# Kernel optimization log

Hardware: AMD Instinct MI355X
Metric: run time of the kernel (lower is better)

The kernel has to match this reference:

```python
import jax, jax.numpy as jnp
import numpy as np

B_IN = 30    # input sphere bandwidth
B_MID = 16   # bandwidth after S2 conv
B_OUT = 10   # bandwidth after SO3 conv
F0, F1 = 100, 100
NUM_CLS = 40
EPS = 1e-5


def _wigner_d(l, betas):
    """Real Wigner-d matrices d^l_{mn}(beta) -> [len(betas), 2l+1, 2l+1] (numpy)."""
    betas = np.asarray(betas, np.float64)
    n = 2 * l + 1
    if l == 0:
        return np.ones((betas.size, 1, 1))
    m = np.arange(-l, l)
    c = np.sqrt(l * (l + 1) - m * (m + 1))      # <m+1|J+|m>
    Jp = np.zeros((n, n)); Jp[np.arange(1, n), np.arange(n - 1)] = c
    K = -(Jp - Jp.T) / 2.0                      # K = -i*Jy, real antisymmetric; d = exp(beta*K)
    w, V = np.linalg.eigh(1j * K)
    ph = np.exp(-1j * np.outer(betas, w))
    return np.einsum('ij,bj,kj->bik', V, ph, V.conj()).real


def _dh(b):
    """Driscoll-Healy beta samples and quadrature weights for bandwidth b."""
    k = np.arange(2 * b)
    beta = np.pi * (2 * k + 1) / (4 * b)
    j = np.arange(b)
    w = (2.0 / b) * np.sin(beta) * (np.sin(np.outer(2 * k + 1, 2 * j + 1) * np.pi / (4 * b)) @ (1.0 / (2 * j + 1)))
    return beta, w


def _project(x, b):
    """Point cloud [B,3,N] -> radial distance image on S2 grid [B,1,2b,2b] (beta, alpha)."""
    nb = 2 * b
    r = jnp.linalg.norm(x, axis=1)                                   # [B,N]
    beta = jnp.arccos(jnp.clip(x[:, 2] / jnp.maximum(r, 1e-8), -1.0, 1.0))
    alpha = jnp.mod(jnp.arctan2(x[:, 1], x[:, 0]), 2.0 * np.pi)
    bi = jnp.clip((beta / np.pi * nb).astype(jnp.int32), 0, nb - 1)
    ai = jnp.clip((alpha / (2.0 * np.pi) * nb).astype(jnp.int32), 0, nb - 1)
    Bb = x.shape[0]
    flat = (jnp.arange(Bb)[:, None] * nb * nb + bi * nb + ai).reshape(-1)
    img = jnp.zeros((Bb * nb * nb,), x.dtype).at[flat].max(r.reshape(-1))
    return img.reshape(Bb, 1, nb, nb)


def _s2_fft(x, b_out):
    """x [B,C,2b,2b] (beta,alpha) -> list over l of fhat^l_m [B,C,2l+1] complex."""
    N = x.shape[-1]
    beta, qw = _dh(N // 2)
    G = jnp.fft.fft(x.astype(jnp.complex64), axis=-1)                # coeff of e^{-im alpha}
    out = []
    for l in range(b_out):
        d0 = _wigner_d(l, beta)[:, :, l]                             # d^l_{m,0}(beta_k)
        wd = jnp.asarray(qw[:, None] * d0 * (2 * np.pi / N), jnp.complex64)
        mi = np.arange(-l, l + 1) % N
        out.append(jnp.einsum('km,bckm->bcm', wd, G[..., mi]))
    return out


def _s2_rft(w, b_out, n_alpha):
    """Dirac kernel on equatorial S2 grid (beta=pi/2) -> list over l of [f_in,f_out,2l+1]."""
    alphas = 2 * np.pi * np.arange(n_alpha) / n_alpha
    wc = w.astype(jnp.complex64) / n_alpha
    out = []
    for l in range(b_out):
        m = np.arange(-l, l + 1)
        basis = _wigner_d(l, [np.pi / 2])[0][:, l][:, None] * np.exp(-1j * np.outer(m, alphas))
        out.append(jnp.einsum('mp,iop->iom', jnp.asarray(basis, jnp.complex64), wc))
    return out


def _so3_fft(x, b_out):
    """x [B,C,2b,2b,2b] (beta,alpha,gamma) -> list over l of [B,C,2l+1,2l+1]."""
    N = x.shape[-1]
    beta, qw = _dh(N // 2)
    G = jnp.fft.fft2(x.astype(jnp.complex64), axes=(-2, -1))
    out = []
    for l in range(b_out):
        d = _wigner_d(l, beta)
        wd = jnp.asarray(qw[:, None, None] * d * (2 * np.pi / N) ** 2, jnp.complex64)
        mi = np.arange(-l, l + 1) % N
        out.append(jnp.einsum('kmn,bckmn->bcmn', wd, G[..., mi[:, None], mi[None, :]]))
    return out


def _so3_rft(w, b_out, n_alpha):
    """Dirac kernel on equatorial SO3 grid (beta=pi/2, gamma=0) -> list of [f_in,f_out,2l+1,2l+1]."""
    alphas = 2 * np.pi * np.arange(n_alpha) / n_alpha
    wc = w.astype(jnp.complex64) / n_alpha
    out = []
    for l in range(b_out):
        m = np.arange(-l, l + 1)
        d = _wigner_d(l, [np.pi / 2])[0]
        basis = d[None] * np.exp(-1j * np.outer(alphas, m))[:, :, None]   # [P,2l+1,2l+1]
        out.append(jnp.einsum('pmn,iop->iomn', jnp.asarray(basis, jnp.complex64), wc))
    return out


def _so3_ifft(Z, b_out):
    """Spectral blocks (list over l of [B,f,2l+1,2l+1]) -> x [B,f,2b,2b,2b] real."""
    N = 2 * b_out
    beta, _ = _dh(b_out)
    Bb, f = Z[0].shape[:2]
    M = jnp.zeros((Bb, f, N, N, N), jnp.complex64)
    for l, Zl in enumerate(Z):
        d = jnp.asarray((2 * l + 1) * _wigner_d(l, beta), jnp.complex64)
        mi = np.arange(-l, l + 1) % N
        M = M.at[:, :, :, mi[:, None], mi[None, :]].add(jnp.einsum('kmn,bfmn->bfkmn', d, Zl))
    return (jnp.fft.ifft2(M, axes=(-2, -1)) * (N * N)).real


def _bn_relu(x, g, b):
    mu = x.mean(axis=(0, 2, 3, 4), keepdims=True)
    var = ((x - mu) ** 2).mean(axis=(0, 2, 3, 4), keepdims=True)
    y = (x - mu) * jax.lax.rsqrt(var + EPS) * g[None, :, None, None, None] + b[None, :, None, None, None]
    return jax.nn.relu(y)


def _so3_integrate(x):
    b = x.shape[-1] // 2
    _, qw = _dh(b)
    return jnp.einsum('bfkag,k->bf', x, jnp.asarray(qw, x.dtype)) * (2 * np.pi / (2 * b)) ** 2


def _forward(x, w_s2, bias_s2, bn1_g, bn1_b, w_so3, bias_so3, bn2_g, bn2_b, lin_w, lin_b):
    img = _project(x, B_IN)                                   # [B,1,60,60]
    X = _s2_fft(img, B_MID)
    Y = _s2_rft(w_s2, B_MID, 2 * B_IN)
    # correlation theorem on S2: Z^l_{mn} = sum_i X^l_{i,m} conj(Y^l_{i,n})
    Z = [jnp.einsum('bim,ion->bomn', Xl, jnp.conj(Yl)) for Xl, Yl in zip(X, Y)]
    h = _so3_ifft(Z, B_MID) + bias_s2[None, :, None, None, None]   # [B,100,32,32,32]
    h = _bn_relu(h, bn1_g, bn1_b)
    X2 = _so3_fft(h, B_OUT)
    Y2 = _so3_rft(w_so3, B_OUT, 2 * B_MID)
    # correlation theorem on SO3: Z^l = X^l @ Y^l^dagger (feature-contracted)
    Z2 = [jnp.einsum('bimk,ionk->bomn', Xl, jnp.conj(Yl)) for Xl, Yl in zip(X2, Y2)]
    h2 = _so3_ifft(Z2, B_OUT) + bias_so3[None, :, None, None, None]  # [B,100,20,20,20]
    h2 = _bn_relu(h2, bn2_g, bn2_b)
    feat = _so3_integrate(h2)                                 # [B,100]
    return feat @ lin_w + lin_b                               # cls_logits [B,40]


def setup_inputs() -> dict:
    key = jax.random.key(0)
    ks = jax.random.split(key, 4)
    B, Np = 8, 1024
    return {
        'x': jax.random.normal(ks[0], (B, 3, Np), jnp.float32),
        'w_s2': jax.random.normal(ks[1], (1, F0, 2 * B_IN), jnp.float32) * 0.1,
        'bias_s2': jnp.zeros((F0,), jnp.float32),
        'bn1_g': jnp.ones((F0,), jnp.float32),
        'bn1_b': jnp.zeros((F0,), jnp.float32),
        'w_so3': jax.random.normal(ks[2], (F0, F1, 2 * B_MID), jnp.float32) * 0.1,
        'bias_so3': jnp.zeros((F1,), jnp.float32),
        'bn2_g': jnp.ones((F1,), jnp.float32),
        'bn2_b': jnp.zeros((F1,), jnp.float32),
        'lin_w': jax.random.normal(ks[3], (F1, NUM_CLS), jnp.float32) * 0.1,
        'lin_b': jnp.zeros((NUM_CLS,), jnp.float32),
    }


def reference(x, w_s2, bias_s2, bn1_g, bn1_b, w_so3, bias_so3, bn2_g, bn2_b, lin_w, lin_b):
    return _forward(x, w_s2, bias_s2, bn1_g, bn1_b, w_so3, bias_so3, bn2_g, bn2_b, lin_w, lin_b)
```

## Files before the change

### kernel.cpp

```cpp
#include <hip/hip_runtime.h>
#include <math.h>

#ifndef M_PI
#define M_PI 3.14159265358979323846
#endif

#define TBL_MAGIC 0x5EED5EEDCAFEF00DULL

__device__ const int c_off2[11] = {0,1,10,35,84,165,286,455,680,969,1330};
__device__ const int c_offH[11] = {0,1,7,22,50,95,161,252,372,525,715};
__device__ const int c_T[17] = {0,1,3,6,10,15,21,28,36,45,55,66,78,91,105,120,136};

__device__ constexpr float CS32[32] = {
  1.0f, 0.98078528f, 0.92387953f, 0.83146961f, 0.70710678f, 0.55557023f, 0.38268343f, 0.19509032f,
  0.0f,-0.19509032f,-0.38268343f,-0.55557023f,-0.70710678f,-0.83146961f,-0.92387953f,-0.98078528f,
 -1.0f,-0.98078528f,-0.92387953f,-0.83146961f,-0.70710678f,-0.55557023f,-0.38268343f,-0.19509032f,
  0.0f, 0.19509032f, 0.38268343f, 0.55557023f, 0.70710678f, 0.83146961f, 0.92387953f, 0.98078528f};
__device__ constexpr float SN32[32] = {
  0.0f, 0.19509032f, 0.38268343f, 0.55557023f, 0.70710678f, 0.83146961f, 0.92387953f, 0.98078528f,
  1.0f, 0.98078528f, 0.92387953f, 0.83146961f, 0.70710678f, 0.55557023f, 0.38268343f, 0.19509032f,
  0.0f,-0.19509032f,-0.38268343f,-0.55557023f,-0.70710678f,-0.83146961f,-0.92387953f,-0.98078528f,
 -1.0f,-0.98078528f,-0.92387953f,-0.83146961f,-0.70710678f,-0.55557023f,-0.38268343f,-0.19509032f};

__device__ __forceinline__ int l_from_sq(int off){ int l=0; while((l+1)*(l+1)<=off) l++; return l; }
__device__ __forceinline__ int l_from_offH(int off){ int l=0; while(c_offH[l+1]<=off) l++; return l; }
__device__ __forceinline__ int l_from_T(int c){ int l=0; while(c_T[l+1]<=c) l++; return l; }

__global__ void k_delta(double* Dd, float* Df, const unsigned long long* __restrict__ tflag){
  if (tflag[0]==TBL_MAGIC) return;
  int l = blockIdx.x; int n = 2*l+1; int n2=n*n;
  __shared__ double A[961], T[961], Tm[961];
  for (int idx=threadIdx.x; idx<n2; idx+=1024){
    int r=idx/n, c=idx-r*n;
    double v=0.0;
    if (r==c+1){ double m=(double)(c-l); v = -0.5*sqrt((double)l*(l+1)-m*(m+1)); }
    else if (c==r+1){ double m=(double)(r-l); v = 0.5*sqrt((double)l*(l+1)-m*(m+1)); }
    A[idx] = v*(M_PI*0.5/128.0);
    T[idx] = (r==c)?1.0:0.0;
  }
  __syncthreads();
  for (int j=14; j>=1; --j){
    for (int idx=threadIdx.x; idx<n2; idx+=1024){
      int r=idx/n, c=idx-r*n; double acc=0.0;
      if (r>0)   acc += A[r*n+(r-1)]*T[(r-1)*n+c];
      if (r<n-1) acc += A[r*n+(r+1)]*T[(r+1)*n+c];
      Tm[idx]=acc;
    }
    __syncthreads();
    for (int idx=threadIdx.x; idx<n2; idx+=1024){
      int r=idx/n, c=idx-r*n;
      T[idx] = ((r==c)?1.0:0.0) + Tm[idx]/(double)j;
    }
    __syncthreads();
  }
  for (int s=0; s<7; ++s){
    for (int idx=threadIdx.x; idx<n2; idx+=1024){
      int r=idx/n, c=idx-r*n; double acc=0.0;
      for (int q=0;q<n;q++) acc += T[r*n+q]*T[q*n+c];
      Tm[idx]=acc;
    }
    __syncthreads();
    for (int idx=threadIdx.x; idx<n2; idx+=1024) T[idx]=Tm[idx];
    __syncthreads();
  }
  for (int idx=threadIdx.x; idx<n2; idx+=1024){ Dd[l*961+idx]=T[idx]; Df[l*961+idx]=(float)T[idx]; }
}

__global__ void k_qw(float* qw30, float* qw16, float* qw10, float2* ph32, float2* ph20, float2* ph60,
                     const unsigned long long* __restrict__ tflag){
  if (tflag[0]==TBL_MAGIC) return;
  int t=threadIdx.x;
  if (t<60){
    double beta=M_PI*(2*t+1)/120.0, s=0.0;
    for (int j=0;j<30;j++) s += sin((double)(2*t+1)*(2*j+1)*M_PI/120.0)/(double)(2*j+1);
    qw30[t]=(float)((2.0/30.0)*sin(beta)*s);
    double a=2.0*M_PI*t/60.0; ph60[t]=make_float2((float)cos(a),(float)sin(a));
  }
  if (t<32){
    double beta=M_PI*(2*t+1)/64.0, s=0.0;
    for (int j=0;j<16;j++) s += sin((double)(2*t+1)*(2*j+1)*M_PI/64.0)/(double)(2*j+1);
    qw16[t]=(float)((2.0/16.0)*sin(beta)*s);
    double a=2.0*M_PI*t/32.0; ph32[t]=make_float2((float)cos(a),(float)sin(a));
  }
  if (t<20){
    double beta=M_PI*(2*t+1)/40.0, s=0.0;
    for (int j=0;j<10;j++) s += sin((double)(2*t+1)*(2*j+1)*M_PI/40.0)/(double)(2*j+1);
    qw10[t]=(float)((2.0/10.0)*sin(beta)*s);
    double a=2.0*M_PI*t/20.0; ph20[t]=make_float2((float)cos(a),(float)sin(a));
  }
}

__global__ void k_tables(const double* Dd, const float* qw30, const float* qw16, const float* qw10,
                         float* wd_s2, float* dif16, float* wd16, float* dif10,
                         const unsigned long long* __restrict__ tflag){
  if (tflag[0]==TBL_MAGIC) return;
  int bid=blockIdx.x;
  __shared__ double cc[32], ss[32];
  int l,k,mode; double beta;
  if (bid<960){ mode=0; l=bid/60; k=bid%60; beta=M_PI*(2*k+1)/120.0; }
  else if (bid<1472){ mode=1; int q=bid-960; l=q/32; k=q%32; beta=M_PI*(2*k+1)/64.0; }
  else { mode=2; int q=bid-1472; l=q/20; k=q%20; beta=M_PI*(2*k+1)/40.0; }
  int n=2*l+1;
  for (int kk=threadIdx.x; kk<=l; kk+=256){ cc[kk]=cos(kk*beta); ss[kk]=sin(kk*beta); }
  __syncthreads();
  const double* D = Dd + l*961;
  if (mode==0){
    for (int mm=threadIdx.x; mm<n; mm+=256){
      int m=mm-l; int p=((m)%4+4)%4; double s=0.0;
      for (int kk=-l; kk<=l; ++kk){
        int ak = kk<0?-kk:kk;
        double c=cc[ak], sn=(kk<0)?-ss[ak]:ss[ak];
        double f=(p==0)?c:(p==1)?sn:(p==2)?-c:-sn;
        s += D[(kk+l)*n+mm]*D[(kk+l)*n+l]*f;
      }
      wd_s2[(l*60+k)*31+mm] = (float)(s*(double)qw30[k]*(2.0*M_PI/60.0));
    }
  } else if (mode==1){
    for (int idx=threadIdx.x; idx<n*n; idx+=256){
      int mm=idx/n, nn=idx-mm*n; int m=mm-l, nb=nn-l;
      int p=((m-nb)%4+4)%4; double s=0.0;
      for (int kk=-l; kk<=l; ++kk){
        int ak = kk<0?-kk:kk;
        double c=cc[ak], sn=(kk<0)?-ss[ak]:ss[ak];
        double f=(p==0)?c:(p==1)?sn:(p==2)?-c:-sn;
        s += D[(kk+l)*n+mm]*D[(kk+l)*n+nn]*f;
      }
      dif16[(size_t)(l*32+k)*961+idx] = (float)((2*l+1)*s);
      if (l<10) wd16[(size_t)(l*32+k)*361+idx] = (float)(s*(double)qw16[k]*(2.0*M_PI/32.0)*(2.0*M_PI/32.0));
    }
  } else {
    for (int idx=threadIdx.x; idx<n*n; idx+=256){
      int mm=idx/n, nn=idx-mm*n; int m=mm-l, nb=nn-l;
      int p=((m-nb)%4+4)%4; double s=0.0;
      for (int kk=-l; kk<=l; ++kk){
        int ak = kk<0?-kk:kk;
        double c=cc[ak], sn=(kk<0)?-ss[ak]:ss[ak];
        double f=(p==0)?c:(p==1)?sn:(p==2)?-c:-sn;
        s += D[(kk+l)*n+mm]*D[(kk+l)*n+nn]*f;
      }
      dif10[(size_t)(l*20+k)*361+idx] = (float)((2*l+1)*s);
    }
  }
}

__global__ void k_setflag(unsigned long long* tflag){ tflag[0]=TBL_MAGIC; }

__global__ void k_project(const float* x, float* img){
  int tid = blockIdx.x*256+threadIdx.x;
  if (tid>=8192) return;
  int b=tid>>10, n=tid&1023;
  float px=x[(b*3+0)*1024+n], py=x[(b*3+1)*1024+n], pz=x[(b*3+2)*1024+n];
  float r = sqrtf(px*px+py*py+pz*pz);
  float rc = fmaxf(r, 1e-8f);
  float ct = fminf(1.f, fmaxf(-1.f, pz/rc));
  float beta = acosf(ct);
  float alpha = atan2f(py, px);
  const float TWO_PI = 6.283185307179586f;
  alpha = fmodf(alpha, TWO_PI); if (alpha<0.f) alpha += TWO_PI;
  int bi = (int)(beta/3.14159265358979323846f*60.f); bi = min(59, max(0, bi));
  int ai = (int)(alpha/TWO_PI*60.f);                 ai = min(59, max(0, ai));
  atomicMax((int*)&img[(b*60+bi)*60+ai], __float_as_int(r));
}

__global__ void k_s2a(const float* __restrict__ img, const float2* __restrict__ ph60, float2* __restrict__ Gg){
  int bid=blockIdx.x; int b=bid/60, k=bid-60*b;
  __shared__ float im[60];
  int t=threadIdx.x;
  if (t<60) im[t]=img[(b*60+k)*60+t];
  __syncthreads();
  if (t<16){
    float sr=0.f, si=0.f;
    for (int a=0;a<60;a++){ float v=im[a]; float2 p=ph60[(t*a)%60]; sr+=v*p.x; si-=v*p.y; }
    Gg[(b*60+k)*16+t]=make_float2(sr,si);
  }
}

__global__ void k_s2b(const float2* __restrict__ Gg, const float* __restrict__ wd_s2, float2* __restrict__ X){
  int b=blockIdx.x;
  __shared__ float2 G[960];
  for (int i=threadIdx.x;i<960;i+=256) G[i]=Gg[b*960+i];
  __syncthreads();
  int off=threadIdx.x;
  int l=0; while((l+1)*(l+1)<=off) l++;
  int mm=off-l*l; int m=mm-l; int am = m<0?-m:m;
  float xr=0.f, xi=0.f;
  for (int k=0;k<60;k++){
    float w=wd_s2[(l*60+k)*31+mm];
    float2 g=G[(k<<4)+am];
    float gi = (m<0)? -g.y : g.y;
    xr += w*g.x; xi += w*gi;
  }
  X[b*256+off]=make_float2(xr,xi);
}

__global__ void k_yc(const float* w_s2, const float* Df, const float2* ph60, float2* YC){
  int f=blockIdx.x; int t=threadIdx.x;
  __shared__ float wv[60];
  __shared__ float2 W[16];
  for (int p=t;p<60;p+=64) wv[p]=w_s2[f*60+p];
  __syncthreads();
  if (t<16){
    float sr=0.f, si=0.f;
    for (int p=0;p<60;p++){ float2 ph=ph60[(t*p)%60]; sr+=wv[p]*ph.x; si-=wv[p]*ph.y; }
    W[t]=make_float2(sr/60.f, si/60.f);
  }
  __syncthreads();
  for (int off=t; off<256; off+=64){
    int l=0; while((l+1)*(l+1)<=off) l++;
    int mm=off-l*l; int m=mm-l; int am=m<0?-m:m;
    float dh=Df[l*961 + mm*(2*l+1) + l];
    float2 wm=W[am];
    float wi = (m>=0)? -wm.y : wm.y;
    YC[f*256+off]=make_float2(dh*wm.x, dh*wi);
  }
}

__global__ void k_u(const float2* X, const float* dif16, const float2* ph32g, float2* u){
  int bid=blockIdx.x;
  int l, k, ns0, ns1;
  if (bid < 256){ l = bid>>5; k = bid&31; ns0=0; ns1=l+1; }
  else {
    int q=bid-256; l = 8 + (q>>6); int half=(q>>5)&1; k=q&31;
    int mid=(l+2)>>1;
    ns0 = half? mid : 0; ns1 = half? (l+1) : mid;
  }
  int n=2*l+1;
  __shared__ float d[961];
  __shared__ float2 Xs[8][31];
  __shared__ float2 ph[32];
  int t=threadIdx.x;
  if (t<32) ph[t]=ph32g[t];
  for (int i=t;i<n*n;i+=256) d[i]=dif16[(size_t)(l*32+k)*961+i];
  if (t<8*n){ int b=t/n, mm=t-b*n; Xs[b][mm]=X[b*256+l*l+mm]; }
  __syncthreads();
  int b=t>>5, a=t&31;
  int base=((b*32+k)*32+a)*136 + c_T[l];
  for (int ns=ns0; ns<ns1; ++ns){
    float ar=0.f, ai=0.f;
    int nn = ns + l;
    for (int mm=0; mm<n; ++mm){
      float2 x=Xs[b][mm];
      float2 p=ph[((mm-l)*a)&31];
      float pr=x.x*p.x-x.y*p.y, pi=x.x*p.y+x.y*p.x;
      float dv=d[mm*n+nn];
      ar += dv*pr; ai += dv*pi;
    }
    u[base+ns]=make_float2(ar,ai);
  }
}

#define KH_F 8
__global__ __launch_bounds__(512,4) void k_h(const float2* __restrict__ u, const float2* __restrict__ YC,
                                             float* __restrict__ h, double2* __restrict__ part){
  int bid=blockIdx.x;
  int fg = bid % 13; int rem = bid/13; int kp = rem & 15; int b = rem >> 4;
  int k0 = kp*2;
  int f0 = fg*KH_F; int F_act = (f0+KH_F<=100)? KH_F : (100-f0);

  __shared__ float2 u2[2][136*33];
  __shared__ float2 ysc[KH_F*136];
  int t=threadIdx.x;

  {
    const float2* ub = u + (size_t)((b*32+k0)*32)*136;
    for (int i=t; i<8704; i+=512){
      int kkl=i/4352, r=i-kkl*4352;
      int a=r/136, c=r-a*136;
      u2[kkl][c*33+a]=ub[i];
    }
  }
  for (int i=t; i<KH_F*136; i+=512){
    int fi=i/136, c=i-fi*136;
    float2 y=make_float2(0.f,0.f);
    if (fi<F_act){
      int l=l_from_T(c); int ns=c-c_T[l];
      y=YC[(size_t)(f0+fi)*256 + l*l+l+ns];
    }
    ysc[i]=y;
  }
  __syncthreads();

  int kk = t>>8, tt = t&255;
  float* vbase = (float*)&u2[kk][0];

  {
    int ns = tt>>4; int sub = tt&15; int ft = sub>>3; int at = sub&7;
    int a0 = at*4;
    const float2* uk = u2[kk];
    float ar[16], ai[16];
    #pragma unroll
    for (int q=0;q<16;q++){ ar[q]=0.f; ai[q]=0.f; }
    for (int l=ns; l<16; ++l){
      int c = c_T[l]+ns;
      float2 y0=ysc[(ft*4+0)*136+c];
      float2 y1=ysc[(ft*4+1)*136+c];
      float2 y2=ysc[(ft*4+2)*136+c];
      float2 y3=ysc[(ft*4+3)*136+c];
      float2 U0=uk[c*33+a0+0];
      float2 U1=uk[c*33+a0+1];
      float2 U2=uk[c*33+a0+2];
      float2 U3=uk[c*33+a0+3];
      #define CM(j,Y,i_,Ui) \
        ar[(j)*4+(i_)] += (Y).x*(Ui).x - (Y).y*(Ui).y; \
        ai[(j)*4+(i_)] += (Y).x*(Ui).y + (Y).y*(Ui).x;
      CM(0,y0,0,U0) CM(0,y0,1,U1) CM(0,y0,2,U2) CM(0,y0,3,U3)
      CM(1,y1,0,U0) CM(1,y1,1,U1) CM(1,y1,2,U2) CM(1,y1,3,U3)
      CM(2,y2,0,U0) CM(2,y2,1,U1) CM(2,y2,2,U2) CM(2,y2,3,U3)
      CM(3,y3,0,U0) CM(3,y3,1,U1) CM(3,y3,2,U2) CM(3,y3,3,U3)
      #undef CM
    }
    __syncthreads();
    float* vr = vbase;
    float* vi = vbase + 4352;
    #pragma unroll
    for (int j=0;j<4;j++){
      #pragma unroll
      for (int i=0;i<4;i++){
        int fi=ft*4+j, a=a0+i;
        vr[(fi*32+a)*17+ns]=ar[j*4+i];
        vi[(fi*32+a)*17+ns]=ai[j*4+i];
      }
    }
  }
  __syncthreads();

  {
    const float* vr = vbase;
    const float* vi = vbase + 4352;
    int fi=tt>>5, a=tt&31;
    float xr[16], xi[16];
    #pragma unroll
    for (int ns=0;ns<16;ns++){ xr[ns]=vr[(fi*32+a)*17+ns]; xi[ns]=vi[(fi*32+a)*17+ns]; }
    float vr0 = xr[0];
    bool wr = (fi<F_act);
    float* hp = h + ((size_t)(b*100+f0+fi)*32 + (k0+kk))*1024 + a;
    float sf=0.f, qf=0.f;
    #pragma unroll
    for (int g=0; g<16; ++g){
      float se=0.f, so=0.f;
      #pragma unroll
      for (int ns=0; ns<16; ++ns){
        const int idx=(ns*g)&31;
        float term = xr[ns]*CS32[idx] - xi[ns]*SN32[idx];
        if (ns & 1) so += term; else se += term;
      }
      float hg  = 2.f*(se+so) - vr0;
      float hg16= 2.f*(se-so) - vr0;
      if (wr){ hp[g*32]=hg; hp[(g+16)*32]=hg16; }
      sf += hg+hg16;
      qf += hg*hg+hg16*hg16;
    }
    for (int d=16; d>0; d>>=1){ sf += __shfl_down(sf, d, 32); qf += __shfl_down(qf, d, 32); }
    if (a==0 && fi<F_act){
      atomicAdd(&part[b*100+f0+fi].x, (double)sf);
      atomicAdd(&part[b*100+f0+fi].y, (double)qf);
    }
  }
}

__global__ void k_bn1(const float* __restrict__ x, int per, double2* __restrict__ partial){
  int bf=blockIdx.x; int t=threadIdx.x;
  const float4* p4=(const float4*)(x + (size_t)bf*per);
  int n4=per>>2;
  double s=0.0, q=0.0;
  for (int i=t;i<n4;i+=256){
    float4 v=p4[i];
    s += (double)v.x+(double)v.y+(double)v.z+(double)v.w;
    q += (double)v.x*v.x+(double)v.y*v.y+(double)v.z*v.z+(double)v.w*v.w;
  }
  __shared__ double rs[256], rq[256];
  rs[t]=s; rq[t]=q; __syncthreads();
  for (int w=128;w>0;w>>=1){ if(t<w){rs[t]+=rs[t+w]; rq[t]+=rq[t+w];} __syncthreads(); }
  if (t==0) partial[bf]=make_double2(rs[0],rq[0]);
}
__global__ void k_bn2(const double2* __restrict__ partial, int per, const float* g, const float* bb,
                      float* scale, float* shift){
  int f=blockIdx.x*64+threadIdx.x;
  if (f>=100) return;
  double s=0.0, q=0.0;
  for (int b=0;b<8;b++){ double2 v=partial[b*100+f]; s+=v.x; q+=v.y; }
  double cnt=8.0*(double)per;
  double mu=s/cnt, var=q/cnt-mu*mu;
  double sc=(double)g[f]/sqrt(var+1e-5);
  scale[f]=(float)sc; shift[f]=(float)((double)bb[f]-mu*sc);
}

template<int M0>
__device__ __forceinline__ void alpha_dft(const float* __restrict__ yk, float2* __restrict__ tdst, int g){
  float ax0=0.f,ay0=0.f, ax1=0.f,ay1=0.f, ax2=0.f,ay2=0.f, ax3=0.f,ay3=0.f, ax4=0.f,ay4=0.f;
  #pragma unroll
  for (int a=0;a<16;a++){
    float ya=yk[a], yb=yk[a+16];
    float yp=ya+yb, ym=ya-yb;
    #define AM(mi, AX, AY) { \
      const int m_ = M0+mi; \
      const int idx_ = (m_*a)&31; \
      float v_ = (m_&1)? ym : yp; \
      AX += v_*CS32[idx_]; \
      AY -= v_*SN32[idx_]; }
    AM(0,ax0,ay0) AM(1,ax1,ay1) AM(2,ax2,ay2) AM(3,ax3,ay3) AM(4,ax4,ay4)
    #undef AM
  }
  tdst[(M0+0)*33+g]=make_float2(ax0,ay0);
  tdst[(M0+1)*33+g]=make_float2(ax1,ay1);
  tdst[(M0+2)*33+g]=make_float2(ax2,ay2);
  tdst[(M0+3)*33+g]=make_float2(ax3,ay3);
  tdst[(M0+4)*33+g]=make_float2(ax4,ay4);
}

__global__ __launch_bounds__(256) void k_g(const float* __restrict__ h, const float* __restrict__ scale,
                                           const float* __restrict__ shift, const float2* __restrict__ ph32g,
                                           float2* __restrict__ G){
  int bid=blockIdx.x; int kq=bid&7; int bc=bid>>3; int c=bc%100;
  int k0 = kq*4;
  __shared__ float y[4][32*33];
  __shared__ float2 tsc[4][10*33];
  int t=threadIdx.x;
  float sc=scale[c], sh=shift[c];
  {
    const float4* h4 = (const float4*)(h + (size_t)bc*32768 + (size_t)k0*1024);
    for (int i=t;i<1024;i+=256){
      float4 v=h4[i];
      int base=i<<2;
      int kk=base>>10, idx=base&1023, g=idx>>5, a=idx&31;
      float* yw=&y[kk][g*33+a];
      yw[0]=fmaxf(v.x*sc+sh, 0.f);
      yw[1]=fmaxf(v.y*sc+sh, 0.f);
      yw[2]=fmaxf(v.z*sc+sh, 0.f);
      yw[3]=fmaxf(v.w*sc+sh, 0.f);
    }
  }
  __syncthreads();
  int wid=t>>6, lane=t&63;
  {
    int mh=wid&1, kh=wid>>1;
    int kk=kh*2+(lane>>5), g=lane&31;
    const float* yk=&y[kk][g*33];
    if (mh==0) alpha_dft<0>(yk, tsc[kk], g);
    else       alpha_dft<5>(yk, tsc[kk], g);
  }
  __syncthreads();
  if (lane<50){
    int kk=wid;
    int mrow=lane/5, p=lane%5;
    int sa=2*p+1, sb=(p==4)? 0 : 2*p+2;
    const float2* tk=&tsc[kk][mrow*33];
    float2 stA=ph32g[sa];
    float2 stB=ph32g[sb];
    float Aa=0.f,Ba=0.f,Ca=0.f,Da=0.f, Ab=0.f,Bb=0.f,Cb=0.f,Db=0.f;
    #pragma unroll
    for (int half=0; half<2; ++half){
      int ea=(sa*half)&3, eb=(sb*half)&3;
      float2 qa=make_float2(ea==0?1.f:(ea==2?-1.f:0.f), ea==1?1.f:(ea==3?-1.f:0.f));
      float2 qb=make_float2(eb==0?1.f:(eb==2?-1.f:0.f), eb==1?1.f:(eb==3?-1.f:0.f));
      #pragma unroll
      for (int g8=0; g8<8; ++g8){
        int g=half*8+g8;
        float2 ta=tk[g], tb=tk[g+16];
        float tpx=ta.x+tb.x, tpy=ta.y+tb.y;
        float tmx=ta.x-tb.x, tmy=ta.y-tb.y;
        Aa += tmx*qa.x; Ba += tmy*qa.y; Ca += tmy*qa.x; Da += tmx*qa.y;
        Ab += tpx*qb.x; Bb += tpy*qb.y; Cb += tpy*qb.x; Db += tpx*qb.y;
        float nax=qa.x*stA.x - qa.y*stA.y, nay=qa.x*stA.y + qa.y*stA.x; qa=make_float2(nax,nay);
        float nbx=qb.x*stB.x - qb.y*stB.y, nby=qb.x*stB.y + qb.y*stB.x; qb=make_float2(nbx,nby);
      }
    }
    float2* Gp = G + (size_t)(bc*32 + k0+kk)*190 + mrow*19;
    Gp[9+sa]=make_float2(Aa+Ba, Ca-Da);
    Gp[9-sa]=make_float2(Aa-Ba, Ca+Da);
    Gp[9+sb]=make_float2(Ab+Bb, Cb-Db);
    Gp[9-sb]=make_float2(Ab-Bb, Cb+Db);
  }
}

__global__ void k_x2(const float2* __restrict__ G, const float* __restrict__ wd16, float2* __restrict__ X2){
  int tid=blockIdx.x*256+threadIdx.x;
  if (tid>=800*715) return;
  int bc=tid/715, i=tid-bc*715;
  int l=l_from_offH(i); int rem=i-c_offH[l]; int n=2*l+1;
  int m=rem/n, kk2=rem-m*n; int ng=kk2-l;
  int j = m*19+(ng+9);
  const float2* Gp = G + (size_t)bc*32*190 + j;
  const float*  wp = wd16 + (size_t)l*32*361 + (m+l)*n + kk2;
  float ar=0.f, ai=0.f;
  #pragma unroll 4
  for (int k=0;k<32;k++){
    float2 gv=Gp[(size_t)k*190];
    float  wv=wp[(size_t)k*361];
    ar += wv*gv.x; ai += wv*gv.y;
  }
  X2[tid]=make_float2(ar, ai);
}

__global__ void k_wh2(const float* w_so3, const float2* ph32g, float2* WH2){
  int tid=blockIdx.x*256+threadIdx.x;
  if (tid>=10000) return;
  int i=tid/100, o=tid-i*100;
  float wv[32];
  for (int p=0;p<32;p++) wv[p]=w_so3[(i*100+o)*32+p];
  for (int m=0;m<10;m++){
    float sr=0.f, si=0.f;
    for (int p=0;p<32;p++){ float2 ph=ph32g[(m*p)&31]; sr+=wv[p]*ph.x; si-=wv[p]*ph.y; }
    WH2[((size_t)m*100+i)*100+o]=make_float2(sr/32.f, si/32.f);
  }
}

__global__ void k_A(const float2* __restrict__ X2, const float* __restrict__ Df, float2* __restrict__ A){
  int tid = blockIdx.x*256 + threadIdx.x;
  if (tid >= 800*715) return;
  int bi = tid/715, off = tid - bi*715;
  int l = l_from_offH(off); int rem = off - c_offH[l]; int n = 2*l+1;
  int m = rem/n, nn = rem - m*n;
  const float2* Xp = X2 + (size_t)bi*715 + c_offH[l] + m*n;
  const float* Dp = Df + l*961 + nn*n;
  float ar=0.f, ai=0.f;
  for (int kk=0; kk<n; ++kk){
    float2 x = Xp[kk]; float dv = Dp[kk];
    ar += x.x*dv; ai += x.y*dv;
  }
  A[tid] = make_float2(ar, ai);
}

__global__ void k_z2(const float2* A, const float2* WH2, float2* Z2){
  int bid=blockIdx.x; int b=bid&7; int r=bid>>3;
  int l=l_from_sq(r); int nn=r-l*l; int n=2*l+1; int ns=nn-l;
  int nrow=l+1;
  __shared__ float2 As[100*10];
  int t=threadIdx.x;
  for (int idx=t; idx<100*nrow; idx+=256){
    int i=idx/nrow, m=idx-i*nrow;
    As[idx]=A[(size_t)(b*100+i)*715 + c_offH[l] + m*n + nn];
  }
  __syncthreads();
  int mabs = ns<0?-ns:ns;
  const float2* Wp = WH2 + (size_t)mabs*10000;
  float sgn = (ns>=0)? -1.f : 1.f;
  for (int idx=t; idx<100*nrow; idx+=256){
    int o=idx/nrow, m=idx-o*nrow;
    float zr=0.f, zi=0.f;
    for (int i=0;i<100;i++){
      float2 a=As[i*nrow+m];
      float2 w=Wp[i*100+o]; float wr=w.x, wi=sgn*w.y;
      zr += a.x*wr - a.y*wi;
      zi += a.x*wi + a.y*wr;
    }
    Z2[(size_t)(b*100+o)*715 + c_offH[l] + m*n + nn]=make_float2(zr,zi);
  }
}

__global__ __launch_bounds__(128) void k_ifft10(const float2* __restrict__ Z2, const float* __restrict__ dif10,
                                                const float2* __restrict__ ph20g, float* __restrict__ h2){
  int bid=blockIdx.x; int bf=bid/20, k=bid-20*bf;
  __shared__ float2 M[190];
  __shared__ float2 T[200];
  __shared__ float2 ph[20];
  int t=threadIdx.x;
  if (t<20) ph[t]=ph20g[t];
  const float2* Zp = Z2 + (size_t)bf*715;
  __syncthreads();
  for (int i=t;i<190;i+=128){
    int ms=i/19, n9=i-ms*19; int nsg=n9-9;
    int a2=nsg<0?-nsg:nsg; int l0 = ms>a2?ms:a2;
    float mr=0.f, mi=0.f;
    for (int l=l0;l<10;l++){
      int n=2*l+1;
      float dv=dif10[(size_t)(l*20+k)*361 + (ms+l)*n+(nsg+l)];
      float2 z=Zp[c_offH[l] + ms*n + (nsg+l)];
      mr += dv*z.x; mi += dv*z.y;
    }
    M[i]=make_float2(mr,mi);
  }
  __syncthreads();
  for (int i=t;i<200;i+=128){
    int ms=i/20, g=i-20*ms;
    const float2* Mp=M+ms*19;
    int idx=(11*g)%20;
    float tr=0.f, ti=0.f;
    #pragma unroll
    for (int n9=0;n9<19;n9++){
      float2 mv=Mp[n9]; float2 p=ph[idx];
      tr += mv.x*p.x - mv.y*p.y;
      ti += mv.x*p.y + mv.y*p.x;
      idx += g; if (idx>=20) idx-=20;
    }
    T[i]=make_float2(tr,ti);
  }
  __syncthreads();
  float* hp = h2 + (size_t)bf*8000 + k*400;
  for (int i=t;i<400;i+=128){
    int a=i/20, g=i-20*a;
    float acc = T[g].x;
    int cur=a;
    #pragma unroll
    for (int ms=1; ms<10; ++ms){
      float2 tv=T[ms*20+g]; float2 p=ph[cur];
      acc += 2.f*(tv.x*p.x - tv.y*p.y);
      cur += a; if (cur>=20) cur-=20;
    }
    hp[i]=acc;
  }
}

__global__ void k_integrate(const float* h2, const float* scale, const float* shift, const float* qw10, float* feat){
  int bf=blockIdx.x; int f=bf%100; int t=threadIdx.x;
  float sc=scale[f], sh=shift[f];
  const float* p=h2+(size_t)bf*8000;
  float s=0.f;
  for (int i=t;i<8000;i+=256){
    float v=fmaxf(p[i]*sc+sh, 0.f);
    s += v*qw10[i/400];
  }
  __shared__ float r[256];
  r[t]=s; __syncthreads();
  for (int w=128;w>0;w>>=1){ if(t<w) r[t]+=r[t+w]; __syncthreads(); }
  if (t==0){
    float c=(float)((2.0*M_PI/20.0)*(2.0*M_PI/20.0));
    feat[bf]=r[0]*c;
  }
}

__global__ void k_logits(const float* feat, const float* lw, const float* lb, float* out){
  int t=blockIdx.x*64+threadIdx.x;
  if (t>=320) return;
  int b=t/40, c=t-40*b;
  float s=lb[c];
  for (int f=0;f<100;f++) s += feat[b*100+f]*lw[f*40+c];
  out[t]=s;
}

extern "C" void kernel_launch(void* const* d_in, const int* in_sizes, int n_in,
                              void* d_out, int out_size, void* d_ws, size_t ws_size,
                              hipStream_t stream){
  (void)in_sizes; (void)n_in; (void)out_size; (void)ws_size;
  const float* x    = (const float*)d_in[0];
  const float* w_s2 = (const float*)d_in[1];
  const float* bn1g = (const float*)d_in[3];
  const float* bn1b = (const float*)d_in[4];
  const float* w_so3= (const float*)d_in[5];
  const float* bn2g = (const float*)d_in[7];
  const float* bn2b = (const float*)d_in[8];
  const float* linw = (const float*)d_in[9];
  const float* linb = (const float*)d_in[10];
  float* out = (float*)d_out;

  char* base=(char*)d_ws; size_t off=0;
  auto alloc=[&](size_t bytes)->void*{ void* p=base+off; off=(off+bytes+255)&~(size_t)255; return p; };
  double* Dd   = (double*)alloc((size_t)16*961*8);
  float*  Df   = (float*) alloc((size_t)16*961*4);
  float*  qw30 = (float*) alloc(256);
  float*  qw16 = (float*) alloc(256);
  float*  qw10 = (float*) alloc(256);
  float2* ph60 = (float2*)alloc(512);
  float2* ph32 = (float2*)alloc(256);
  float2* ph20 = (float2*)alloc(256);
  float*  wd_s2= (float*) alloc((size_t)16*60*31*4);
  float*  dif16= (float*) alloc((size_t)16*32*961*4);
  float*  wd16 = (float*) alloc((size_t)10*32*361*4);
  float*  dif10= (float*) alloc((size_t)10*20*361*4);
  float*  img  = (float*) alloc((size_t)8*3600*4);
  float2* Gg   = (float2*)alloc((size_t)8*960*8);
  float2* X    = (float2*)alloc((size_t)8*256*8);
  float2* YC   = (float2*)alloc((size_t)100*256*8);
  float2* u    = (float2*)alloc((size_t)8*32*32*136*8);
  float*  h    = (float*) alloc((size_t)8*100*32768*4);
  float*  sc1  = (float*) alloc(512);
  float*  sh1  = (float*) alloc(512);
  float2* Gbuf = (float2*)alloc((size_t)800*32*190*8);
  float2* X2   = (float2*)alloc((size_t)800*715*8);
  float2* WH2  = (float2*)alloc((size_t)10*100*100*8);
  float2* A    = (float2*)alloc((size_t)800*715*8);
  float2* Z2   = (float2*)alloc((size_t)800*715*8);
  float*  h2   = (float*) alloc((size_t)8*100*8000*4);
  float*  sc2  = (float*) alloc(512);
  float*  sh2  = (float*) alloc(512);
  float*  feat = (float*) alloc(4096);
  double2* part= (double2*)alloc((size_t)800*16);
  unsigned long long* tflag = (unsigned long long*)alloc(256);

  k_delta<<<16, 1024, 0, stream>>>(Dd, Df, tflag);
  k_qw<<<1, 64, 0, stream>>>(qw30, qw16, qw10, ph32, ph20, ph60, tflag);
  k_tables<<<1672, 256, 0, stream>>>(Dd, qw30, qw16, qw10, wd_s2, dif16, wd16, dif10, tflag);
  k_setflag<<<1, 1, 0, stream>>>(tflag);
  hipMemsetAsync(img, 0, (size_t)8*3600*4, stream);
  hipMemsetAsync(part, 0, (size_t)800*16, stream);
  k_project<<<32, 256, 0, stream>>>(x, img);
  k_s2a<<<480, 64, 0, stream>>>(img, ph60, Gg);
  k_s2b<<<8, 256, 0, stream>>>(Gg, wd_s2, X);
  k_yc<<<100, 64, 0, stream>>>(w_s2, Df, ph60, YC);
  k_u<<<768, 256, 0, stream>>>(X, dif16, ph32, u);
  k_h<<<8*16*13, 512, 0, stream>>>(u, YC, h, part);
  k_bn2<<<2, 64, 0, stream>>>(part, 32768, bn1g, bn1b, sc1, sh1);
  k_g<<<800*8, 256, 0, stream>>>(h, sc1, sh1, ph32, Gbuf);
  k_x2<<<(800*715+255)/256, 256, 0, stream>>>(Gbuf, wd16, X2);
  k_wh2<<<40, 256, 0, stream>>>(w_so3, ph32, WH2);
  k_A<<<(800*715+255)/256, 256, 0, stream>>>(X2, Df, A);
  k_z2<<<800, 256, 0, stream>>>(A, WH2, Z2);
  k_ifft10<<<16000, 128, 0, stream>>>(Z2, dif10, ph20, h2);
  k_bn1<<<800, 256, 0, stream>>>(h2, 8000, part);
  k_bn2<<<2, 64, 0, stream>>>(part, 8000, bn2g, bn2b, sc2, sh2);
  k_integrate<<<800, 256, 0, stream>>>(h2, sc2, sh2, qw10, feat);
  k_logits<<<5, 64, 0, stream>>>(feat, linw, linb, out);
}
```

Measured before the change: 474.8 us.

## Store u in padded transposed layout and tile k_z2 weights in shared memory

The producer kernel now writes u directly in the padded [c][33] layout that k_h uses in shared memory, so k_h can load it with contiguous float4 copies instead of a scattered transposing copy with integer divisions. Separately, k_z2 is restructured to stage 25-row chunks of the weight matrix in shared memory, with each thread accumulating up to five m outputs in registers. This removes repeated uncoalesced global weight reads. The trade-off is strided global writes in the producer and more shared memory in k_z2.

```diff
diff --git a/kernel.cpp b/kernel.cpp
--- a/kernel.cpp
+++ b/kernel.cpp
@@ -234,7 +234,7 @@
   if (t<8*n){ int b=t/n, mm=t-b*n; Xs[b][mm]=X[b*256+l*l+mm]; }
   __syncthreads();
   int b=t>>5, a=t&31;
-  int base=((b*32+k)*32+a)*136 + c_T[l];
+  float2* up = u + (size_t)(b*32+k)*4488 + a;
   for (int ns=ns0; ns<ns1; ++ns){
     float ar=0.f, ai=0.f;
     int nn = ns + l;
@@ -245,7 +245,7 @@
       float dv=d[mm*n+nn];
       ar += dv*pr; ai += dv*pi;
     }
-    u[base+ns]=make_float2(ar,ai);
+    up[(size_t)(c_T[l]+ns)*33]=make_float2(ar,ai);
   }
 }
 
@@ -257,17 +257,14 @@
   int k0 = kp*2;
   int f0 = fg*KH_F; int F_act = (f0+KH_F<=100)? KH_F : (100-f0);
 
-  __shared__ float2 u2[2][136*33];
+  __shared__ alignas(16) float2 u2[2][4488];
   __shared__ float2 ysc[KH_F*136];
   int t=threadIdx.x;
 
   {
-    const float2* ub = u + (size_t)((b*32+k0)*32)*136;
-    for (int i=t; i<8704; i+=512){
-      int kkl=i/4352, r=i-kkl*4352;
-      int a=r/136, c=r-a*136;
-      u2[kkl][c*33+a]=ub[i];
-    }
+    const float4* gs = (const float4*)(u + (size_t)(b*32+k0)*4488);
+    float4* ls = (float4*)&u2[0][0];
+    for (int j=t; j<4488; j+=512) ls[j]=gs[j];
   }
   for (int i=t; i<KH_F*136; i+=512){
     int fi=i/136, c=i-fi*136;
@@ -521,30 +518,55 @@
   A[tid] = make_float2(ar, ai);
 }
 
-__global__ void k_z2(const float2* A, const float2* WH2, float2* Z2){
+__global__ __launch_bounds__(256) void k_z2(const float2* A, const float2* WH2, float2* Z2){
   int bid=blockIdx.x; int b=bid&7; int r=bid>>3;
   int l=l_from_sq(r); int nn=r-l*l; int n=2*l+1; int ns=nn-l;
   int nrow=l+1;
-  __shared__ float2 As[100*10];
+  __shared__ float2 As[1000];
+  __shared__ float2 Ws[2500];
   int t=threadIdx.x;
   for (int idx=t; idx<100*nrow; idx+=256){
     int i=idx/nrow, m=idx-i*nrow;
     As[idx]=A[(size_t)(b*100+i)*715 + c_offH[l] + m*n + nn];
   }
-  __syncthreads();
   int mabs = ns<0?-ns:ns;
   const float2* Wp = WH2 + (size_t)mabs*10000;
   float sgn = (ns>=0)? -1.f : 1.f;
-  for (int idx=t; idx<100*nrow; idx+=256){
-    int o=idx/nrow, m=idx-o*nrow;
-    float zr=0.f, zi=0.f;
-    for (int i=0;i<100;i++){
-      float2 a=As[i*nrow+m];
-      float2 w=Wp[i*100+o]; float wr=w.x, wi=sgn*w.y;
-      zr += a.x*wr - a.y*wi;
-      zi += a.x*wi + a.y*wr;
-    }
-    Z2[(size_t)(b*100+o)*715 + c_offH[l] + m*n + nn]=make_float2(zr,zi);
+  int o = t>>1, p = t&1;
+  bool act = (t<200);
+  float2 acc[5];
+  #pragma unroll
+  for (int q=0;q<5;q++) acc[q]=make_float2(0.f,0.f);
+  for (int c0=0; c0<100; c0+=25){
+    __syncthreads();
+    for (int idx=t; idx<2500; idx+=256){
+      Ws[idx]=Wp[(size_t)c0*100 + idx];
+    }
+    __syncthreads();
+    if (act){
+      for (int ii=0; ii<25; ++ii){
+        float2 w = Ws[ii*100+o];
+        float wr=w.x, wi=sgn*w.y;
+        const float2* ap = &As[(c0+ii)*nrow];
+        #pragma unroll
+        for (int q=0;q<5;q++){
+          int m = p + 2*q;
+          if (m<nrow){
+            float2 a=ap[m];
+            acc[q].x += a.x*wr - a.y*wi;
+            acc[q].y += a.x*wi + a.y*wr;
+          }
+        }
+      }
+    }
+  }
+  if (act){
+    float2* Zp = Z2 + (size_t)(b*100+o)*715 + c_offH[l] + nn;
+    #pragma unroll
+    for (int q=0;q<5;q++){
+      int m=p+2*q;
+      if (m<nrow) Zp[(size_t)m*n]=acc[q];
+    }
   }
 }
 
@@ -661,7 +683,7 @@
   float2* Gg   = (float2*)alloc((size_t)8*960*8);
   float2* X    = (float2*)alloc((size_t)8*256*8);
   float2* YC   = (float2*)alloc((size_t)100*256*8);
-  float2* u    = (float2*)alloc((size_t)8*32*32*136*8);
+  float2* u    = (float2*)alloc((size_t)8*32*4488*8);
   float*  h    = (float*) alloc((size_t)8*100*32768*4);
   float*  sc1  = (float*) alloc(512);
   float*  sh1  = (float*) alloc(512);
```

Result: no change. 476.8 us (+0.4%).

## Store u in padded transposed layout, stage G in LDS, fuse BN2 stats

Applied to the files above, without the earlier changes.

k_u now writes u directly in the padded column-major [c][a] layout (stride 33) that k_h wants, so k_h can load its tile with plain float4 copies instead of a scattered transpose. k_x2 is restructured to one block per batch-channel, staging the 32x190 G slab in shared memory so the weight-times-G reduction reads from LDS. The second BN statistics pass (k_bn1) is folded into k_ifft10 through a block reduction and double atomics on a re-zeroed partial buffer, which saves one full read of h2. In exchange, k_u's global stores become strided, and the statistics now go through 16000 atomic-add pairs.

```diff
diff --git a/kernel.cpp b/kernel.cpp
--- a/kernel.cpp
+++ b/kernel.cpp
@@ -234,7 +234,7 @@
   if (t<8*n){ int b=t/n, mm=t-b*n; Xs[b][mm]=X[b*256+l*l+mm]; }
   __syncthreads();
   int b=t>>5, a=t&31;
-  int base=((b*32+k)*32+a)*136 + c_T[l];
+  float2* up = u + (size_t)(b*32+k)*4488 + a;
   for (int ns=ns0; ns<ns1; ++ns){
     float ar=0.f, ai=0.f;
     int nn = ns + l;
@@ -245,7 +245,7 @@
       float dv=d[mm*n+nn];
       ar += dv*pr; ai += dv*pi;
     }
-    u[base+ns]=make_float2(ar,ai);
+    up[(size_t)(c_T[l]+ns)*33]=make_float2(ar,ai);
   }
 }
 
@@ -257,17 +257,14 @@
   int k0 = kp*2;
   int f0 = fg*KH_F; int F_act = (f0+KH_F<=100)? KH_F : (100-f0);
 
-  __shared__ float2 u2[2][136*33];
+  __shared__ alignas(16) float2 u2[2][4488];
   __shared__ float2 ysc[KH_F*136];
   int t=threadIdx.x;
 
   {
-    const float2* ub = u + (size_t)((b*32+k0)*32)*136;
-    for (int i=t; i<8704; i+=512){
-      int kkl=i/4352, r=i-kkl*4352;
-      int a=r/136, c=r-a*136;
-      u2[kkl][c*33+a]=ub[i];
-    }
+    const float4* gs = (const float4*)(u + (size_t)(b*32+k0)*4488);
+    float4* ls = (float4*)&u2[0][0];
+    for (int j=t; j<4488; j+=512) ls[j]=gs[j];
   }
   for (int i=t; i<KH_F*136; i+=512){
     int fi=i/136, c=i-fi*136;
@@ -358,21 +355,6 @@
   }
 }
 
-__global__ void k_bn1(const float* __restrict__ x, int per, double2* __restrict__ partial){
-  int bf=blockIdx.x; int t=threadIdx.x;
-  const float4* p4=(const float4*)(x + (size_t)bf*per);
-  int n4=per>>2;
-  double s=0.0, q=0.0;
-  for (int i=t;i<n4;i+=256){
-    float4 v=p4[i];
-    s += (double)v.x+(double)v.y+(double)v.z+(double)v.w;
-    q += (double)v.x*v.x+(double)v.y*v.y+(double)v.z*v.z+(double)v.w*v.w;
-  }
-  __shared__ double rs[256], rq[256];
-  rs[t]=s; rq[t]=q; __syncthreads();
-  for (int w=128;w>0;w>>=1){ if(t<w){rs[t]+=rs[t+w]; rq[t]+=rq[t+w];} __syncthreads(); }
-  if (t==0) partial[bf]=make_double2(rs[0],rq[0]);
-}
 __global__ void k_bn2(const double2* __restrict__ partial, int per, const float* g, const float* bb,
                       float* scale, float* shift){
   int f=blockIdx.x*64+threadIdx.x;
@@ -473,23 +455,27 @@
   }
 }
 
-__global__ void k_x2(const float2* __restrict__ G, const float* __restrict__ wd16, float2* __restrict__ X2){
-  int tid=blockIdx.x*256+threadIdx.x;
-  if (tid>=800*715) return;
-  int bc=tid/715, i=tid-bc*715;
-  int l=l_from_offH(i); int rem=i-c_offH[l]; int n=2*l+1;
-  int m=rem/n, kk2=rem-m*n; int ng=kk2-l;
-  int j = m*19+(ng+9);
-  const float2* Gp = G + (size_t)bc*32*190 + j;
-  const float*  wp = wd16 + (size_t)l*32*361 + (m+l)*n + kk2;
-  float ar=0.f, ai=0.f;
-  #pragma unroll 4
-  for (int k=0;k<32;k++){
-    float2 gv=Gp[(size_t)k*190];
-    float  wv=wp[(size_t)k*361];
-    ar += wv*gv.x; ai += wv*gv.y;
-  }
-  X2[tid]=make_float2(ar, ai);
+__global__ __launch_bounds__(256) void k_x2(const float2* __restrict__ G, const float* __restrict__ wd16,
+                                            float2* __restrict__ X2){
+  int bc=blockIdx.x;
+  __shared__ float2 Gs[32*190];
+  int t=threadIdx.x;
+  for (int idx=t; idx<6080; idx+=256) Gs[idx]=G[(size_t)bc*6080+idx];
+  __syncthreads();
+  for (int i=t; i<715; i+=256){
+    int l=l_from_offH(i); int rem=i-c_offH[l]; int n=2*l+1;
+    int m=rem/n, kk2=rem-m*n; int ng=kk2-l;
+    int j = m*19+(ng+9);
+    const float* wp = wd16 + (size_t)l*32*361 + (m+l)*n + kk2;
+    float ar=0.f, ai=0.f;
+    #pragma unroll 4
+    for (int k=0;k<32;k++){
+      float2 gv=Gs[k*190+j];
+      float  wv=wp[(size_t)k*361];
+      ar += wv*gv.x; ai += wv*gv.y;
+    }
+    X2[(size_t)bc*715+i]=make_float2(ar, ai);
+  }
 }
 
 __global__ void k_wh2(const float* w_so3, const float2* ph32g, float2* WH2){
@@ -549,11 +535,13 @@
 }
 
 __global__ __launch_bounds__(128) void k_ifft10(const float2* __restrict__ Z2, const float* __restrict__ dif10,
-                                                const float2* __restrict__ ph20g, float* __restrict__ h2){
+                                                const float2* __restrict__ ph20g, float* __restrict__ h2,
+                                                double2* __restrict__ part){
   int bid=blockIdx.x; int bf=bid/20, k=bid-20*bf;
   __shared__ float2 M[190];
   __shared__ float2 T[200];
   __shared__ float2 ph[20];
+  __shared__ float rs[128], rq[128];
   int t=threadIdx.x;
   if (t<20) ph[t]=ph20g[t];
   const float2* Zp = Z2 + (size_t)bf*715;
@@ -587,6 +575,7 @@
   }
   __syncthreads();
   float* hp = h2 + (size_t)bf*8000 + k*400;
+  float sf=0.f, qf=0.f;
   for (int i=t;i<400;i+=128){
     int a=i/20, g=i-20*a;
     float acc = T[g].x;
@@ -598,6 +587,13 @@
       cur += a; if (cur>=20) cur-=20;
     }
     hp[i]=acc;
+    sf += acc; qf += acc*acc;
+  }
+  rs[t]=sf; rq[t]=qf; __syncthreads();
+  for (int w=64;w>0;w>>=1){ if(t<w){rs[t]+=rs[t+w]; rq[t]+=rq[t+w];} __syncthreads(); }
+  if (t==0){
+    atomicAdd(&part[bf].x, (double)rs[0]);
+    atomicAdd(&part[bf].y, (double)rq[0]);
   }
 }
 
@@ -661,7 +657,7 @@
   float2* Gg   = (float2*)alloc((size_t)8*960*8);
   float2* X    = (float2*)alloc((size_t)8*256*8);
   float2* YC   = (float2*)alloc((size_t)100*256*8);
-  float2* u    = (float2*)alloc((size_t)8*32*32*136*8);
+  float2* u    = (float2*)alloc((size_t)8*32*4488*8);
   float*  h    = (float*) alloc((size_t)8*100*32768*4);
   float*  sc1  = (float*) alloc(512);
   float*  sh1  = (float*) alloc(512);
@@ -690,13 +686,13 @@
   k_u<<<768, 256, 0, stream>>>(X, dif16, ph32, u);
   k_h<<<8*16*13, 512, 0, stream>>>(u, YC, h, part);
   k_bn2<<<2, 64, 0, stream>>>(part, 32768, bn1g, bn1b, sc1, sh1);
+  hipMemsetAsync(part, 0, (size_t)800*16, stream);
   k_g<<<800*8, 256, 0, stream>>>(h, sc1, sh1, ph32, Gbuf);
-  k_x2<<<(800*715+255)/256, 256, 0, stream>>>(Gbuf, wd16, X2);
+  k_x2<<<800, 256, 0, stream>>>(Gbuf, wd16, X2);
   k_wh2<<<40, 256, 0, stream>>>(w_so3, ph32, WH2);
   k_A<<<(800*715+255)/256, 256, 0, stream>>>(X2, Df, A);
   k_z2<<<800, 256, 0, stream>>>(A, WH2, Z2);
-  k_ifft10<<<16000, 128, 0, stream>>>(Z2, dif10, ph20, h2);
-  k_bn1<<<800, 256, 0, stream>>>(h2, 8000, part);
+  k_ifft10<<<16000, 128, 0, stream>>>(Z2, dif10, ph20, h2, part);
   k_bn2<<<2, 64, 0, stream>>>(part, 8000, bn2g, bn2b, sc2, sh2);
   k_integrate<<<800, 256, 0, stream>>>(h2, sc2, sh2, qw10, feat);
   k_logits<<<5, 64, 0, stream>>>(feat, linw, linb, out);
```

After: 508.7 us. 1.07x slower.
